# Optimization experiments

Measured on AMD Instinct MI355X. Metric: run time of the kernel, lower is better.

## Reference

```python
import jax, jax.numpy as jnp
import numpy as np

N_NODES = 50000
N_EDGES = 600000
D = 128


def setup_inputs() -> dict:
    key = jax.random.key(0)
    k1, k2, k3, k4, k5, k6 = jax.random.split(key, 6)
    h = jax.random.normal(k1, (N_NODES, D), dtype=jnp.float32)
    e_h = jax.random.normal(k2, (N_EDGES, D), dtype=jnp.float32)
    norm = jax.random.uniform(k3, (N_NODES, 1), dtype=jnp.float32)
    dst = jax.random.randint(k4, (N_EDGES,), 0, N_NODES)
    # nn.Linear(in_hid=128, out_hid=128) weight/bias
    W = jax.random.normal(k5, (D, D), dtype=jnp.float32) * (1.0 / np.sqrt(D))
    b = jax.random.normal(k6, (D,), dtype=jnp.float32) * 0.01
    return {"h": h, "e_h": e_h, "norm": norm, "dst": dst, "W": W, "b": b}


def reference(h, e_h, norm, dst, W, b):
    # DGL fn.v_mul_e: message per edge = h[dst] * e_h  (elementwise)
    msg = h[dst] * e_h                                    # [E, D]
    # fn.sum: scatter-sum messages to destination nodes
    agg = jax.ops.segment_sum(msg, dst, num_segments=N_NODES)  # [N, D]
    # apply_func: linear projection, then per-node norm scaling
    out = agg @ W.T + b                                   # [N, D]
    out = out * norm                                      # broadcast [N,1]
    # dropout is identity in eval mode; activation is None by default
    return out
```

## Files before the change

kernel.cpp:

```cpp
#include <hip/hip_runtime.h>

#define N_NODES 50000
#define N_EDGES 600000
#define D 128
#define TILE_N 32
#define SCAN_B 1024
#define N_SCAN_BLOCKS ((N_NODES + SCAN_B - 1) / SCAN_B)

typedef float f4 __attribute__((ext_vector_type(4)));


__global__ __launch_bounds__(256) void hist_kernel(
    const int* __restrict__ dst, int* __restrict__ cnt)
{
    int e = blockIdx.x * 256 + threadIdx.x;
    if (e < N_EDGES) atomicAdd(&cnt[dst[e]], 1);
}

__global__ __launch_bounds__(SCAN_B) void scan_kernel(
    const int* __restrict__ cnt, unsigned long long* __restrict__ desc,
    int* __restrict__ offsets, int* __restrict__ cursor)
{
    const int t  = threadIdx.x;
    const int bx = blockIdx.x;
    const int i  = bx * SCAN_B + t;
    const int v  = (i < N_NODES) ? cnt[i] : 0;

    const int lane = t & 63;
    const int w    = t >> 6;
    int incl = v;
#pragma unroll
    for (int s = 1; s < 64; s <<= 1) {
        int u = __shfl_up(incl, s, 64);
        if (lane >= s) incl += u;
    }
    __shared__ int wsum[SCAN_B / 64];
    if (lane == 63) wsum[w] = incl;
    __syncthreads();
    if (t < SCAN_B / 64) {
        int x = wsum[t];
#pragma unroll
        for (int s = 1; s < SCAN_B / 64; s <<= 1) {
            int u = __shfl_up(x, s, SCAN_B / 64);
            if (t >= s) x += u;
        }
        wsum[t] = x;
    }
    __syncthreads();
    const int block_total   = wsum[SCAN_B / 64 - 1];
    const int excl_in_block = (w ? wsum[w - 1] : 0) + (incl - v);

    if (t == 0)
        __hip_atomic_store(&desc[bx],
            (unsigned long long)(unsigned)block_total | (1ull << 63),
            __ATOMIC_RELEASE, __HIP_MEMORY_SCOPE_AGENT);

    __shared__ int base_sh;
    if (t < 64) {
        int pred = 0;
        if (t < bx) {
            unsigned long long e;
            do {
                e = __hip_atomic_load(&desc[t], __ATOMIC_ACQUIRE,
                                      __HIP_MEMORY_SCOPE_AGENT);
            } while (!(e >> 63));
            pred = (int)(unsigned)e;
        }
#pragma unroll
        for (int s = 32; s > 0; s >>= 1) pred += __shfl_down(pred, s, 64);
        if (t == 0) base_sh = pred;
    }
    __syncthreads();

    const int excl = base_sh + excl_in_block;
    if (i < N_NODES) { offsets[i] = excl; cursor[i] = excl; }
    if (i == N_NODES - 1) offsets[N_NODES] = excl + v;
}

__global__ __launch_bounds__(256) void fill_kernel(
    const int* __restrict__ dst, int* __restrict__ cursor,
    int* __restrict__ edge_ids)
{
    int e = blockIdx.x * 256 + threadIdx.x;
    if (e < N_EDGES) {
        int pos = atomicAdd(&cursor[dst[e]], 1);
        edge_ids[pos] = e;
    }
}

__global__ __launch_bounds__(256) void agg_kernel(
    const float* __restrict__ h, const float* __restrict__ e_h,
    const int* __restrict__ offsets, const int* __restrict__ edge_ids,
    float* __restrict__ A)
{
    int gid  = blockIdx.x * 256 + threadIdx.x;
    int node = gid >> 5;
    int lane = gid & 31;
    if (node >= N_NODES) return;

    const int beg = offsets[node];
    const int end = offsets[node + 1];
    const int fo  = lane << 2;

    f4 acc = (f4){0.f, 0.f, 0.f, 0.f};

    for (int c = beg; c < end; c += 32) {
        const int rem = end - c;
        const int cap = rem < 32 ? rem : 32;
        int myid = (lane < cap) ? edge_ids[c + lane] : 0;

        int j = 0;
        const int cap4 = cap & ~3;
        for (; j < cap4; j += 4) {
            int id0 = __shfl(myid, j + 0, 32);
            int id1 = __shfl(myid, j + 1, 32);
            int id2 = __shfl(myid, j + 2, 32);
            int id3 = __shfl(myid, j + 3, 32);
            f4 v0 = __builtin_nontemporal_load((const f4*)(e_h + (size_t)id0 * D + fo));
            f4 v1 = __builtin_nontemporal_load((const f4*)(e_h + (size_t)id1 * D + fo));
            f4 v2 = __builtin_nontemporal_load((const f4*)(e_h + (size_t)id2 * D + fo));
            f4 v3 = __builtin_nontemporal_load((const f4*)(e_h + (size_t)id3 * D + fo));
            acc += (v0 + v1) + (v2 + v3);
        }
        for (; j < cap; ++j) {
            int id = __shfl(myid, j, 32);
            f4 v = __builtin_nontemporal_load((const f4*)(e_h + (size_t)id * D + fo));
            acc += v;
        }
    }

    f4 hv = *(const f4*)(h + (size_t)node * D + fo);
    acc *= hv;
    *(f4*)(A + (size_t)node * D + fo) = acc;
}

__global__ __launch_bounds__(256, 2) void gemm_from_A(
    const float* __restrict__ A, const float* __restrict__ norm,
    const float* __restrict__ W, const float* __restrict__ b,
    float* __restrict__ out)
{
    __shared__ float Wl[D * D];
    __shared__ float Al[TILE_N * D];
    const int tid = threadIdx.x;
    const int n0  = blockIdx.x * TILE_N;

    for (int it = 0; it < 16; ++it) {
        int group = it * 256 + tid;
        int c  = group >> 5;
        int kg = group & 31;
        float4 wv = *(const float4*)(W + (size_t)c * D + (kg << 2));
        int g = (kg + c) & 31;
        *(float4*)(Wl + c * D + (g << 2)) = wv;
    }
    for (int it = 0; it < 4; ++it) {
        int group = it * 256 + tid;
        int nl = group >> 5;
        int f  = (group & 31) << 2;
        int n  = n0 + nl;
        float4 a = make_float4(0.f, 0.f, 0.f, 0.f);
        if (n < N_NODES) a = *(const float4*)(A + (size_t)n * D + f);
        *(float4*)(Al + nl * D + f) = a;
    }
    __syncthreads();

    const int cg = tid & 31;
    const int ng = tid >> 5;
    float facc[4][4];
#pragma unroll
    for (int i = 0; i < 4; ++i)
#pragma unroll
        for (int j = 0; j < 4; ++j) facc[i][j] = 0.f;

#pragma unroll 4
    for (int kc = 0; kc < 32; ++kc) {
        float4 a[4];
#pragma unroll
        for (int i = 0; i < 4; ++i)
            a[i] = *(const float4*)(Al + (ng * 4 + i) * D + (kc << 2));
        float4 w[4];
#pragma unroll
        for (int j = 0; j < 4; ++j) {
            int c = cg + 32 * j;
            int g = (kc + c) & 31;
            w[j] = *(const float4*)(Wl + c * D + (g << 2));
        }
#pragma unroll
        for (int i = 0; i < 4; ++i)
#pragma unroll
            for (int j = 0; j < 4; ++j)
                facc[i][j] += a[i].x * w[j].x + a[i].y * w[j].y +
                              a[i].z * w[j].z + a[i].w * w[j].w;
    }
    float bias[4];
#pragma unroll
    for (int j = 0; j < 4; ++j) bias[j] = b[cg + 32 * j];
#pragma unroll
    for (int i = 0; i < 4; ++i) {
        int n = n0 + ng * 4 + i;
        if (n >= N_NODES) break;
        float nv = norm[n];
#pragma unroll
        for (int j = 0; j < 4; ++j)
            out[(size_t)n * D + cg + 32 * j] = (facc[i][j] + bias[j]) * nv;
    }
}

__global__ __launch_bounds__(256) void scatter_kernel(
    const float* __restrict__ e_h, const int* __restrict__ dst,
    float* __restrict__ S)
{
    long long idx = (long long)blockIdx.x * 256 + threadIdx.x;
    int edge = (int)(idx >> 5);
    if (edge >= N_EDGES) return;
    int f = ((int)idx & 31) << 2;
    const float4 v = *(const float4*)(e_h + (size_t)edge * D + f);
    float* p = S + (size_t)dst[edge] * D + f;
    atomicAdd(p + 0, v.x);
    atomicAdd(p + 1, v.y);
    atomicAdd(p + 2, v.z);
    atomicAdd(p + 3, v.w);
}

__global__ __launch_bounds__(256, 2) void gemm_kernel(
    const float* __restrict__ h, const float* __restrict__ S,
    const float* __restrict__ norm, const float* __restrict__ W,
    const float* __restrict__ b, float* __restrict__ out)
{
    __shared__ float Wl[D * D];
    __shared__ float Al[TILE_N * D];
    const int tid = threadIdx.x;
    const int n0  = blockIdx.x * TILE_N;

    for (int it = 0; it < 16; ++it) {
        int group = it * 256 + tid;
        int c  = group >> 5;
        int kg = group & 31;
        float4 wv = *(const float4*)(W + (size_t)c * D + (kg << 2));
        int g = (kg + c) & 31;
        *(float4*)(Wl + c * D + (g << 2)) = wv;
    }
    for (int it = 0; it < 4; ++it) {
        int group = it * 256 + tid;
        int nl = group >> 5;
        int f  = (group & 31) << 2;
        int n  = n0 + nl;
        float4 a = make_float4(0.f, 0.f, 0.f, 0.f);
        if (n < N_NODES) {
            float4 hv = *(const float4*)(h + (size_t)n * D + f);
            float4 sv = *(const float4*)(S + (size_t)n * D + f);
            a = make_float4(hv.x * sv.x, hv.y * sv.y, hv.z * sv.z, hv.w * sv.w);
        }
        *(float4*)(Al + nl * D + f) = a;
    }
    __syncthreads();

    const int cg = tid & 31;
    const int ng = tid >> 5;
    float facc[4][4];
#pragma unroll
    for (int i = 0; i < 4; ++i)
#pragma unroll
        for (int j = 0; j < 4; ++j) facc[i][j] = 0.f;

#pragma unroll 4
    for (int kc = 0; kc < 32; ++kc) {
        float4 a[4];
#pragma unroll
        for (int i = 0; i < 4; ++i)
            a[i] = *(const float4*)(Al + (ng * 4 + i) * D + (kc << 2));
        float4 w[4];
#pragma unroll
        for (int j = 0; j < 4; ++j) {
            int c = cg + 32 * j;
            int g = (kc + c) & 31;
            w[j] = *(const float4*)(Wl + c * D + (g << 2));
        }
#pragma unroll
        for (int i = 0; i < 4; ++i)
#pragma unroll
            for (int j = 0; j < 4; ++j)
                facc[i][j] += a[i].x * w[j].x + a[i].y * w[j].y +
                              a[i].z * w[j].z + a[i].w * w[j].w;
    }
    float bias[4];
#pragma unroll
    for (int j = 0; j < 4; ++j) bias[j] = b[cg + 32 * j];
#pragma unroll
    for (int i = 0; i < 4; ++i) {
        int n = n0 + ng * 4 + i;
        if (n >= N_NODES) break;
        float nv = norm[n];
#pragma unroll
        for (int j = 0; j < 4; ++j)
            out[(size_t)n * D + cg + 32 * j] = (facc[i][j] + bias[j]) * nv;
    }
}

extern "C" void kernel_launch(void* const* d_in, const int* in_sizes, int n_in,
                              void* d_out, int out_size, void* d_ws, size_t ws_size,
                              hipStream_t stream) {
    const float* h    = (const float*)d_in[0];
    const float* e_h  = (const float*)d_in[1];
    const float* norm = (const float*)d_in[2];
    const int*   dst  = (const int*)d_in[3];
    const float* W    = (const float*)d_in[4];
    const float* b    = (const float*)d_in[5];
    float* out = (float*)d_out;

    const size_t ints_needed = (size_t)N_NODES + 128 + (N_NODES + 1) + N_EDGES;
    const size_t full_bytes  = ints_needed * sizeof(int)
                             + (size_t)N_NODES * D * sizeof(float);

    if (ws_size >= full_bytes) {
        int* cursor   = (int*)d_ws;
        unsigned long long* desc = (unsigned long long*)(cursor + N_NODES);
        int* offsets  = cursor + N_NODES + 128;
        int* edge_ids = offsets + N_NODES + 1;
        float* A      = (float*)(edge_ids + N_EDGES);

        hipMemsetAsync(cursor, 0, ((size_t)N_NODES + 128) * sizeof(int), stream);

        int eblocks = (N_EDGES + 255) / 256;
        hist_kernel<<<eblocks, 256, 0, stream>>>(dst, cursor);
        scan_kernel<<<N_SCAN_BLOCKS, SCAN_B, 0, stream>>>(cursor, desc,
                                                          offsets, cursor);
        fill_kernel<<<eblocks, 256, 0, stream>>>(dst, cursor, edge_ids);

        int ablocks = ((N_NODES * 32) + 255) / 256;
        agg_kernel<<<ablocks, 256, 0, stream>>>(h, e_h, offsets, edge_ids, A);

        int gblocks = (N_NODES + TILE_N - 1) / TILE_N;
        gemm_from_A<<<gblocks, 256, 0, stream>>>(A, norm, W, b, out);
    } else {
        const size_t s_bytes = (size_t)N_NODES * D * sizeof(float);
        float* S = (ws_size >= s_bytes) ? (float*)d_ws : out;
        hipMemsetAsync(S, 0, s_bytes, stream);
        int scatter_blocks = (N_EDGES * 32 + 255) / 256;
        scatter_kernel<<<scatter_blocks, 256, 0, stream>>>(e_h, dst, S);
        int gemm_blocks = (N_NODES + TILE_N - 1) / TILE_N;
        gemm_kernel<<<gemm_blocks, 256, 0, stream>>>(h, S, norm, W, b, out);
    }
}
```

Baseline: 172.0 us.

## Fuse histogram, scan, fill and aggregation into one persistent kernel with grid barriers

Replaces four separate launches (histogram, decoupled-lookback scan, CSR fill, aggregation) with one persistent kernel of 1792 blocks that uses software grid barriers between phases. Each thread keeps its dst values in registers across the histogram and fill phases, and the scan now handles 4 nodes per thread with 256-thread blocks. Aggregation becomes a grid-stride loop over nodes. This removes launch gaps and one re-read of dst, at the cost of spin-wait barriers whose correctness depends on all 1792 blocks being co-resident.

```diff
diff --git a/kernel.cpp b/kernel.cpp
--- a/kernel.cpp
+++ b/kernel.cpp
@@ -6,132 +6,148 @@
 #define TILE_N 32
 #define SCAN_B 1024
 #define N_SCAN_BLOCKS ((N_NODES + SCAN_B - 1) / SCAN_B)
+#define NBLK 1792
 
 typedef float f4 __attribute__((ext_vector_type(4)));
 
 
-__global__ __launch_bounds__(256) void hist_kernel(
-    const int* __restrict__ dst, int* __restrict__ cnt)
-{
-    int e = blockIdx.x * 256 + threadIdx.x;
-    if (e < N_EDGES) atomicAdd(&cnt[dst[e]], 1);
-}
-
-__global__ __launch_bounds__(SCAN_B) void scan_kernel(
-    const int* __restrict__ cnt, unsigned long long* __restrict__ desc,
-    int* __restrict__ offsets, int* __restrict__ cursor)
-{
-    const int t  = threadIdx.x;
-    const int bx = blockIdx.x;
-    const int i  = bx * SCAN_B + t;
-    const int v  = (i < N_NODES) ? cnt[i] : 0;
-
-    const int lane = t & 63;
-    const int w    = t >> 6;
-    int incl = v;
-#pragma unroll
-    for (int s = 1; s < 64; s <<= 1) {
-        int u = __shfl_up(incl, s, 64);
-        if (lane >= s) incl += u;
-    }
-    __shared__ int wsum[SCAN_B / 64];
-    if (lane == 63) wsum[w] = incl;
+__device__ __forceinline__ void grid_barrier(int* bar, int nblk) {
     __syncthreads();
-    if (t < SCAN_B / 64) {
-        int x = wsum[t];
-#pragma unroll
-        for (int s = 1; s < SCAN_B / 64; s <<= 1) {
-            int u = __shfl_up(x, s, SCAN_B / 64);
-            if (t >= s) x += u;
-        }
-        wsum[t] = x;
+    if (threadIdx.x == 0) {
+        __hip_atomic_fetch_add(bar, 1, __ATOMIC_ACQ_REL,
+                               __HIP_MEMORY_SCOPE_AGENT);
+        while (__hip_atomic_load(bar, __ATOMIC_ACQUIRE,
+                                 __HIP_MEMORY_SCOPE_AGENT) < nblk)
+            __builtin_amdgcn_s_sleep(2);
     }
     __syncthreads();
-    const int block_total   = wsum[SCAN_B / 64 - 1];
-    const int excl_in_block = (w ? wsum[w - 1] : 0) + (incl - v);
-
-    if (t == 0)
-        __hip_atomic_store(&desc[bx],
-            (unsigned long long)(unsigned)block_total | (1ull << 63),
-            __ATOMIC_RELEASE, __HIP_MEMORY_SCOPE_AGENT);
-
-    __shared__ int base_sh;
-    if (t < 64) {
-        int pred = 0;
-        if (t < bx) {
-            unsigned long long e;
-            do {
-                e = __hip_atomic_load(&desc[t], __ATOMIC_ACQUIRE,
-                                      __HIP_MEMORY_SCOPE_AGENT);
-            } while (!(e >> 63));
-            pred = (int)(unsigned)e;
-        }
-#pragma unroll
-        for (int s = 32; s > 0; s >>= 1) pred += __shfl_down(pred, s, 64);
-        if (t == 0) base_sh = pred;
-    }
-    __syncthreads();
-
-    const int excl = base_sh + excl_in_block;
-    if (i < N_NODES) { offsets[i] = excl; cursor[i] = excl; }
-    if (i == N_NODES - 1) offsets[N_NODES] = excl + v;
-}
-
-__global__ __launch_bounds__(256) void fill_kernel(
-    const int* __restrict__ dst, int* __restrict__ cursor,
-    int* __restrict__ edge_ids)
-{
-    int e = blockIdx.x * 256 + threadIdx.x;
-    if (e < N_EDGES) {
-        int pos = atomicAdd(&cursor[dst[e]], 1);
-        edge_ids[pos] = e;
-    }
-}
-
-__global__ __launch_bounds__(256) void agg_kernel(
+}
+
+__global__ __launch_bounds__(256, 8) void build_and_agg(
     const float* __restrict__ h, const float* __restrict__ e_h,
-    const int* __restrict__ offsets, const int* __restrict__ edge_ids,
+    const int* __restrict__ dst,
+    int* __restrict__ cnt,
+    unsigned long long* __restrict__ desc,
+    int* __restrict__ bar,
+    int* __restrict__ offsets, int* __restrict__ edge_ids,
     float* __restrict__ A)
 {
-    int gid  = blockIdx.x * 256 + threadIdx.x;
-    int node = gid >> 5;
-    int lane = gid & 31;
-    if (node >= N_NODES) return;
-
-    const int beg = offsets[node];
-    const int end = offsets[node + 1];
-    const int fo  = lane << 2;
-
-    f4 acc = (f4){0.f, 0.f, 0.f, 0.f};
-
-    for (int c = beg; c < end; c += 32) {
-        const int rem = end - c;
-        const int cap = rem < 32 ? rem : 32;
-        int myid = (lane < cap) ? edge_ids[c + lane] : 0;
-
-        int j = 0;
-        const int cap4 = cap & ~3;
-        for (; j < cap4; j += 4) {
-            int id0 = __shfl(myid, j + 0, 32);
-            int id1 = __shfl(myid, j + 1, 32);
-            int id2 = __shfl(myid, j + 2, 32);
-            int id3 = __shfl(myid, j + 3, 32);
-            f4 v0 = __builtin_nontemporal_load((const f4*)(e_h + (size_t)id0 * D + fo));
-            f4 v1 = __builtin_nontemporal_load((const f4*)(e_h + (size_t)id1 * D + fo));
-            f4 v2 = __builtin_nontemporal_load((const f4*)(e_h + (size_t)id2 * D + fo));
-            f4 v3 = __builtin_nontemporal_load((const f4*)(e_h + (size_t)id3 * D + fo));
-            acc += (v0 + v1) + (v2 + v3);
-        }
-        for (; j < cap; ++j) {
-            int id = __shfl(myid, j, 32);
-            f4 v = __builtin_nontemporal_load((const f4*)(e_h + (size_t)id * D + fo));
-            acc += v;
-        }
-    }
-
-    f4 hv = *(const f4*)(h + (size_t)node * D + fo);
-    acc *= hv;
-    *(f4*)(A + (size_t)node * D + fo) = acc;
+    const int tid  = threadIdx.x;
+    const int bid  = blockIdx.x;
+    const int gtid = bid * 256 + tid;
+    const int nthr = NBLK * 256;
+
+    __shared__ int wsum2[4];
+    __shared__ int wpre[4];
+    __shared__ int base_sh;
+
+    const int e0 = gtid;
+    const int e1 = gtid + nthr;
+    int d0 = -1, d1 = -1;
+    if (e0 < N_EDGES) { d0 = dst[e0]; atomicAdd(&cnt[d0], 1); }
+    if (e1 < N_EDGES) { d1 = dst[e1]; atomicAdd(&cnt[d1], 1); }
+    grid_barrier(bar + 0, NBLK);
+
+    if (bid < N_SCAN_BLOCKS) {
+        const int i0 = bid * SCAN_B + tid * 4;
+        int v[4];
+#pragma unroll
+        for (int k = 0; k < 4; ++k) {
+            int idx = i0 + k;
+            v[k] = (idx < N_NODES) ? cnt[idx] : 0;
+        }
+        const int s    = v[0] + v[1] + v[2] + v[3];
+        const int lane = tid & 63;
+        const int w    = tid >> 6;
+        int incl = s;
+#pragma unroll
+        for (int sh = 1; sh < 64; sh <<= 1) {
+            int u = __shfl_up(incl, sh, 64);
+            if (lane >= sh) incl += u;
+        }
+        if (lane == 63) wsum2[w] = incl;
+        __syncthreads();
+        if (tid == 0) {
+            int acc = 0;
+#pragma unroll
+            for (int k = 0; k < 4; ++k) { wpre[k] = acc; acc += wsum2[k]; }
+            wsum2[0] = acc;
+        }
+        __syncthreads();
+        const int block_total = wsum2[0];
+        if (tid == 0)
+            __hip_atomic_store(&desc[bid],
+                (unsigned long long)(unsigned)block_total | (1ull << 63),
+                __ATOMIC_RELEASE, __HIP_MEMORY_SCOPE_AGENT);
+        if (tid < 64) {
+            int pred = 0;
+            if (tid < bid) {
+                unsigned long long dv;
+                do {
+                    dv = __hip_atomic_load(&desc[tid], __ATOMIC_ACQUIRE,
+                                           __HIP_MEMORY_SCOPE_AGENT);
+                } while (!(dv >> 63));
+                pred = (int)(unsigned)dv;
+            }
+#pragma unroll
+            for (int sh = 32; sh > 0; sh >>= 1)
+                pred += __shfl_down(pred, sh, 64);
+            if (tid == 0) base_sh = pred;
+        }
+        __syncthreads();
+        int excl = base_sh + wpre[w] + (incl - s);
+#pragma unroll
+        for (int k = 0; k < 4; ++k) {
+            int idx = i0 + k;
+            if (idx < N_NODES) {
+                offsets[idx] = excl;
+                cnt[idx]     = excl;
+                if (idx == N_NODES - 1) offsets[N_NODES] = excl + v[k];
+            }
+            excl += v[k];
+        }
+    }
+    grid_barrier(bar + 16, NBLK);
+
+    if (e0 < N_EDGES) { int p = atomicAdd(&cnt[d0], 1); edge_ids[p] = e0; }
+    if (e1 < N_EDGES) { int p = atomicAdd(&cnt[d1], 1); edge_ids[p] = e1; }
+    grid_barrier(bar + 32, NBLK);
+
+    const int grp  = tid >> 5;
+    const int lane = tid & 31;
+    const int fo   = lane << 2;
+    for (int n = bid * 8 + grp; n < N_NODES; n += NBLK * 8) {
+        const int beg = offsets[n];
+        const int end = offsets[n + 1];
+        f4 acc = (f4){0.f, 0.f, 0.f, 0.f};
+        for (int c = beg; c < end; c += 32) {
+            const int rem = end - c;
+            const int cap = rem < 32 ? rem : 32;
+            int myid = (lane < cap) ? edge_ids[c + lane] : 0;
+
+            int j = 0;
+            const int cap4 = cap & ~3;
+            for (; j < cap4; j += 4) {
+                int id0 = __shfl(myid, j + 0, 32);
+                int id1 = __shfl(myid, j + 1, 32);
+                int id2 = __shfl(myid, j + 2, 32);
+                int id3 = __shfl(myid, j + 3, 32);
+                f4 v0 = __builtin_nontemporal_load((const f4*)(e_h + (size_t)id0 * D + fo));
+                f4 v1 = __builtin_nontemporal_load((const f4*)(e_h + (size_t)id1 * D + fo));
+                f4 v2 = __builtin_nontemporal_load((const f4*)(e_h + (size_t)id2 * D + fo));
+                f4 v3 = __builtin_nontemporal_load((const f4*)(e_h + (size_t)id3 * D + fo));
+                acc += (v0 + v1) + (v2 + v3);
+            }
+            for (; j < cap; ++j) {
+                int id = __shfl(myid, j, 32);
+                f4 v = __builtin_nontemporal_load((const f4*)(e_h + (size_t)id * D + fo));
+                acc += v;
+            }
+        }
+        f4 hv = *(const f4*)(h + (size_t)n * D + fo);
+        acc *= hv;
+        *(f4*)(A + (size_t)n * D + fo) = acc;
+    }
 }
 
 __global__ __launch_bounds__(256, 2) void gemm_from_A(
@@ -307,27 +323,24 @@
     const float* b    = (const float*)d_in[5];
     float* out = (float*)d_out;
 
-    const size_t ints_needed = (size_t)N_NODES + 128 + (N_NODES + 1) + N_EDGES;
-    const size_t full_bytes  = ints_needed * sizeof(int)
-                             + (size_t)N_NODES * D * sizeof(float);
+    const size_t HEAD_INTS = (size_t)N_NODES + 128 + 64;
+    const size_t A_OFF_INTS =
+        ((HEAD_INTS + (N_NODES + 1) + N_EDGES + 3) / 4) * 4;
+    const size_t full_bytes = A_OFF_INTS * sizeof(int)
+                            + (size_t)N_NODES * D * sizeof(float);
 
     if (ws_size >= full_bytes) {
         int* cursor   = (int*)d_ws;
         unsigned long long* desc = (unsigned long long*)(cursor + N_NODES);
-        int* offsets  = cursor + N_NODES + 128;
+        int* bar      = (int*)(desc + 64);
+        int* offsets  = bar + 64;
         int* edge_ids = offsets + N_NODES + 1;
-        float* A      = (float*)(edge_ids + N_EDGES);
-
-        hipMemsetAsync(cursor, 0, ((size_t)N_NODES + 128) * sizeof(int), stream);
-
-        int eblocks = (N_EDGES + 255) / 256;
-        hist_kernel<<<eblocks, 256, 0, stream>>>(dst, cursor);
-        scan_kernel<<<N_SCAN_BLOCKS, SCAN_B, 0, stream>>>(cursor, desc,
-                                                          offsets, cursor);
-        fill_kernel<<<eblocks, 256, 0, stream>>>(dst, cursor, edge_ids);
-
-        int ablocks = ((N_NODES * 32) + 255) / 256;
-        agg_kernel<<<ablocks, 256, 0, stream>>>(h, e_h, offsets, edge_ids, A);
+        float* A      = (float*)((int*)d_ws + A_OFF_INTS);
+
+        hipMemsetAsync(cursor, 0, HEAD_INTS * sizeof(int), stream);
+
+        build_and_agg<<<NBLK, 256, 0, stream>>>(h, e_h, dst, cursor, desc,
+                                                bar, offsets, edge_ids, A);
 
         int gblocks = (N_NODES + TILE_N - 1) / TILE_N;
         gemm_from_A<<<gblocks, 256, 0, stream>>>(A, norm, W, b, out);
```

After: 529.1 us. 208% more time.
